# Optimization experiments

Hardware: AMD Instinct MI355X
Metric: run time of the kernel (lower is better)

Reference implementation:

```python
import jax, jax.numpy as jnp
import numpy as np

U, S, D = 4096, 8192, 32
NUM_REGIONS = 128
GA = 0.1


def setup_inputs() -> dict:
    key = jax.random.key(0)
    k1, k2, k3, k4, k5, k6 = jax.random.split(key, 6)
    user_emb = jax.random.normal(k1, (U, D), dtype=jnp.float32) * 0.01
    item_emb = jax.random.normal(k2, (S, D), dtype=jnp.float32) * 0.01
    train_mask = jax.random.randint(k3, (U, S), 0, 2, dtype=jnp.int32)
    true_qos = jax.random.normal(k4, (U, S), dtype=jnp.float32)
    us_lossweight = jax.random.uniform(k5, (U, S), dtype=jnp.float32)
    region_index = jax.random.randint(k6, (U,), 0, NUM_REGIONS, dtype=jnp.int32)
    return {
        "user_emb": user_emb,
        "item_emb": item_emb,
        "train_mask": train_mask,
        "true_qos": true_qos,
        "us_lossweight": us_lossweight,
        "region_index": region_index,
    }


def _region_loss(user_emb, region_index):
    # per-region sums and counts via a single segment reduction
    sums = jax.ops.segment_sum(user_emb, region_index, num_segments=NUM_REGIONS)  # [R, D]
    counts = jax.ops.segment_sum(jnp.ones((user_emb.shape[0],), dtype=user_emb.dtype),
                                 region_index, num_segments=NUM_REGIONS)  # [R]
    cnt = counts[region_index]                      # [U]
    loo_mean = (sums[region_index] - user_emb) / jnp.maximum(cnt - 1.0, 1.0)[:, None]
    dev = jnp.abs(user_emb - loo_mean)              # [U, D]
    # regions with a single user are skipped in the original loop
    valid = (cnt > 1.0)[:, None]
    return jnp.sum(jnp.where(valid, dev, 0.0))


def reference(user_emb, item_emb, train_mask, true_qos, us_lossweight, region_index):
    pre_qos = (user_emb @ item_emb.T) * train_mask.astype(user_emb.dtype)  # [U, S]
    mse = (pre_qos - true_qos) ** 2
    loss = jnp.sum(us_lossweight * mse)
    regionloss = _region_loss(user_emb, region_index)
    return loss + GA * regionloss
```

## Files before the change

kernel.cpp:

```cpp
#include <hip/hip_runtime.h>

#define U 4096
#define S 8192
#define D 32
#define NUM_REGIONS 128
#define GA 0.1f

#define TU 32
#define TI 512
#define THREADS 256
#define LCAP 256


__global__ __launch_bounds__(256) void region_kernel(
    const float* __restrict__ user_emb,
    const int* __restrict__ region_index,
    float* __restrict__ rl_accum) {
    __shared__ int   ridx[U];
    __shared__ int   ulist[LCAP];
    __shared__ int   ucnt;
    __shared__ float part[8][D];
    __shared__ float redsum[D];

    if (threadIdx.x == 0) ucnt = 0;

    #pragma unroll
    for (int i = 0; i < U / 4 / 256; i++)
        ((int4*)ridx)[threadIdx.x + i * 256] =
            ((const int4*)region_index)[threadIdx.x + i * 256];
    __syncthreads();

    const int r = blockIdx.x;

    for (int u = threadIdx.x; u < U; u += 256) {
        if (ridx[u] == r) {
            int p = atomicAdd(&ucnt, 1);
            if (p < LCAP) ulist[p] = u;
        }
    }
    __syncthreads();

    const int n = min(ucnt, LCAP);
    const int d = threadIdx.x & (D - 1);
    const int w = threadIdx.x >> 5;

    float psum = 0.0f;
    for (int i = w; i < n; i += 8)
        psum += user_emb[ulist[i] * D + d];
    part[w][d] = psum;
    __syncthreads();
    if (w == 0) {
        float s = 0.0f;
        #pragma unroll
        for (int i = 0; i < 8; i++) s += part[i][d];
        redsum[d] = s;
    }
    __syncthreads();

    float acc = 0.0f;
    if (n > 1) {
        const float inv = 1.0f / (float)(n - 1);
        const float sd = redsum[d];
        for (int i = w; i < n; i += 8) {
            float e = user_emb[ulist[i] * D + d];
            acc += fabsf(e - (sd - e) * inv);
        }
    }

    #pragma unroll
    for (int off = 32; off > 0; off >>= 1) acc += __shfl_down(acc, off, 64);
    __shared__ float wp[4];
    int lane = threadIdx.x & 63, wid = threadIdx.x >> 6;
    if (lane == 0) wp[wid] = acc;
    __syncthreads();
    if (threadIdx.x == 0)
        atomicAdd(rl_accum, wp[0] + wp[1] + wp[2] + wp[3]);
}


#define PIN4(v) asm volatile("" : "+v"(v.x), "+v"(v.y), "+v"(v.z), "+v"(v.w))

__global__ __attribute__((amdgpu_waves_per_eu(4, 4)))
void mse_kernel(
    const float* __restrict__ user_emb,
    const float* __restrict__ item_emb,
    const int* __restrict__ train_mask,
    const float* __restrict__ true_qos,
    const float* __restrict__ us_lossweight,
    float* __restrict__ loss_accum) {
    __shared__ float uemb[TU][D];

    const int ub = blockIdx.x * TU;
    const int sb = blockIdx.y * TI;

    {
        const float4* src = (const float4*)(user_emb + (size_t)ub * D);
        ((float4*)&uemb[0][0])[threadIdx.x] = src[threadIdx.x];
    }

    const int s0 = sb + 2 * threadIdx.x;

    float4 ir0[8], ir1[8];
    {
        const float4* ip0 = (const float4*)(item_emb + (size_t)s0 * D);
        const float4* ip1 = (const float4*)(item_emb + (size_t)(s0 + 1) * D);
        #pragma unroll
        for (int k = 0; k < 8; k++) { ir0[k] = ip0[k]; ir1[k] = ip1[k]; }
        #pragma unroll
        for (int k = 0; k < 8; k++) { PIN4(ir0[k]); PIN4(ir1[k]); }
    }
    __syncthreads();

    const size_t base0 = (size_t)ub * S + s0;
    int2   m_n = *(const int2*)(train_mask + base0);
    float2 q_n = *(const float2*)(true_qos + base0);
    float2 w_n = *(const float2*)(us_lossweight + base0);

    float acc = 0.0f;
    #pragma unroll 1
    for (int uu = 0; uu < TU; uu++) {
        int2   m = m_n;
        float2 q = q_n;
        float2 w = w_n;
        if (uu + 1 < TU) {
            const size_t nb = base0 + (size_t)(uu + 1) * S;
            m_n = *(const int2*)(train_mask + nb);
            q_n = *(const float2*)(true_qos + nb);
            w_n = *(const float2*)(us_lossweight + nb);
        }

        float d0 = 0.0f, d1 = 0.0f;
        const float4* ur = (const float4*)&uemb[uu][0];
        #pragma unroll
        for (int k = 0; k < 8; k++) {
            float4 uv = ur[k];
            d0 += uv.x * ir0[k].x + uv.y * ir0[k].y + uv.z * ir0[k].z + uv.w * ir0[k].w;
            d1 += uv.x * ir1[k].x + uv.y * ir1[k].y + uv.z * ir1[k].z + uv.w * ir1[k].w;
        }
        float p0 = d0 * (float)m.x;
        float p1 = d1 * (float)m.y;
        float e0 = p0 - q.x;
        float e1 = p1 - q.y;
        acc += w.x * e0 * e0 + w.y * e1 * e1;
    }

    #pragma unroll
    for (int off = 32; off > 0; off >>= 1) acc += __shfl_down(acc, off, 64);
    __shared__ float wp[THREADS / 64];
    int lane = threadIdx.x & 63, wid = threadIdx.x >> 6;
    if (lane == 0) wp[wid] = acc;
    __syncthreads();
    if (threadIdx.x == 0) {
        float t = 0.0f;
        #pragma unroll
        for (int i = 0; i < THREADS / 64; i++) t += wp[i];
        atomicAdd(loss_accum, t);
    }
}

__global__ void finalize_kernel(const float* __restrict__ loss_acc,
                                const float* __restrict__ rl_acc,
                                float* __restrict__ out) {
    out[0] = loss_acc[0] + GA * rl_acc[0];
}

extern "C" void kernel_launch(void* const* d_in, const int* in_sizes, int n_in,
                              void* d_out, int out_size, void* d_ws, size_t ws_size,
                              hipStream_t stream) {
    const float* user_emb      = (const float*)d_in[0];
    const float* item_emb      = (const float*)d_in[1];
    const int*   train_mask    = (const int*)d_in[2];
    const float* true_qos      = (const float*)d_in[3];
    const float* us_lossweight = (const float*)d_in[4];
    const int*   region_index  = (const int*)d_in[5];
    float* out = (float*)d_out;

    float* ws       = (float*)d_ws;
    float* loss_acc = ws;
    float* rl_acc   = ws + 1;
    hipMemsetAsync(d_ws, 0, 2 * sizeof(float), stream);

    region_kernel<<<NUM_REGIONS, 256, 0, stream>>>(user_emb, region_index, rl_acc);

    dim3 grid(U / TU, S / TI);
    mse_kernel<<<grid, THREADS, 0, stream>>>(
        user_emb, item_emb, train_mask, true_qos, us_lossweight, loss_acc);

    finalize_kernel<<<1, 1, 0, stream>>>(loss_acc, rl_acc, out);
}
```

Before: 376.9 us.

## Fuse region loss into MSE kernel and process one item per thread

Merges the region-loss kernel into the MSE kernel: blocks with blockIdx.y==0 (128 of them, one per region since U/TU=128) run the region reduction after their MSE tile, which removes one kernel launch. Each thread now handles a single item instead of two, and TI is halved to keep the grid covering all items. The waves_per_eu(4,4) attribute is replaced by launch_bounds. The fused kernel carries the 16KB ridx shared array in every block, which may reduce occupancy, and the scalar loads replace the earlier int2/float2 vector loads.

```diff
diff --git a/kernel.cpp b/kernel.cpp
--- a/kernel.cpp
+++ b/kernel.cpp
@@ -7,30 +7,102 @@
 #define GA 0.1f
 
 #define TU 32
-#define TI 512
+#define TI 256
 #define THREADS 256
 #define LCAP 256
 
+#define PIN4(v) asm volatile("" : "+v"(v.x), "+v"(v.y), "+v"(v.z), "+v"(v.w))
 
-__global__ __launch_bounds__(256) void region_kernel(
+
+__global__ __launch_bounds__(THREADS) void fused_kernel(
     const float* __restrict__ user_emb,
+    const float* __restrict__ item_emb,
+    const int* __restrict__ train_mask,
+    const float* __restrict__ true_qos,
+    const float* __restrict__ us_lossweight,
     const int* __restrict__ region_index,
+    float* __restrict__ loss_accum,
     float* __restrict__ rl_accum) {
+    __shared__ float uemb[TU][D];
     __shared__ int   ridx[U];
     __shared__ int   ulist[LCAP];
     __shared__ int   ucnt;
     __shared__ float part[8][D];
     __shared__ float redsum[D];
+    __shared__ float wp[THREADS / 64];
+
+    const int ub = blockIdx.x * TU;
+    const int sb = blockIdx.y * TI;
+
+    {
+        const float4* src = (const float4*)(user_emb + (size_t)ub * D);
+        ((float4*)&uemb[0][0])[threadIdx.x] = src[threadIdx.x];
+    }
+
+    const int s0 = sb + threadIdx.x;
+    float4 ir[8];
+    {
+        const float4* ip = (const float4*)(item_emb + (size_t)s0 * D);
+        #pragma unroll
+        for (int k = 0; k < 8; k++) ir[k] = ip[k];
+        #pragma unroll
+        for (int k = 0; k < 8; k++) PIN4(ir[k]);
+    }
+    __syncthreads();
+
+    const size_t base0 = (size_t)ub * S + s0;
+    int   m_n = train_mask[base0];
+    float q_n = true_qos[base0];
+    float w_n = us_lossweight[base0];
+
+    float acc = 0.0f;
+    #pragma unroll 1
+    for (int uu = 0; uu < TU; uu++) {
+        int   m = m_n;
+        float q = q_n;
+        float w = w_n;
+        if (uu + 1 < TU) {
+            const size_t nb = base0 + (size_t)(uu + 1) * S;
+            m_n = train_mask[nb];
+            q_n = true_qos[nb];
+            w_n = us_lossweight[nb];
+        }
+
+        float d0 = 0.0f;
+        const float4* ur = (const float4*)&uemb[uu][0];
+        #pragma unroll
+        for (int k = 0; k < 8; k++) {
+            float4 uv = ur[k];
+            d0 += uv.x * ir[k].x + uv.y * ir[k].y + uv.z * ir[k].z + uv.w * ir[k].w;
+        }
+        float p = d0 * (float)m;
+        float e = p - q;
+        acc += w * e * e;
+    }
+
+    #pragma unroll
+    for (int off = 32; off > 0; off >>= 1) acc += __shfl_down(acc, off, 64);
+    {
+        int lane = threadIdx.x & 63, wid = threadIdx.x >> 6;
+        if (lane == 0) wp[wid] = acc;
+        __syncthreads();
+        if (threadIdx.x == 0) {
+            float t = 0.0f;
+            #pragma unroll
+            for (int i = 0; i < THREADS / 64; i++) t += wp[i];
+            atomicAdd(loss_accum, t);
+        }
+    }
+
+    if (blockIdx.y != 0) return;
+    const int r = blockIdx.x;
 
     if (threadIdx.x == 0) ucnt = 0;
-
     #pragma unroll
     for (int i = 0; i < U / 4 / 256; i++)
         ((int4*)ridx)[threadIdx.x + i * 256] =
             ((const int4*)region_index)[threadIdx.x + i * 256];
     __syncthreads();
-
-    const int r = blockIdx.x;
 
     for (int u = threadIdx.x; u < U; u += 256) {
         if (ridx[u] == r) {
@@ -42,119 +114,43 @@
 
     const int n = min(ucnt, LCAP);
     const int d = threadIdx.x & (D - 1);
-    const int w = threadIdx.x >> 5;
+    const int w8 = threadIdx.x >> 5;
 
     float psum = 0.0f;
-    for (int i = w; i < n; i += 8)
+    for (int i = w8; i < n; i += 8)
         psum += user_emb[ulist[i] * D + d];
-    part[w][d] = psum;
+    part[w8][d] = psum;
     __syncthreads();
-    if (w == 0) {
-        float s = 0.0f;
+    if (w8 == 0) {
+        float sum = 0.0f;
         #pragma unroll
-        for (int i = 0; i < 8; i++) s += part[i][d];
-        redsum[d] = s;
+        for (int i = 0; i < 8; i++) sum += part[i][d];
+        redsum[d] = sum;
     }
     __syncthreads();
 
-    float acc = 0.0f;
+    float racc = 0.0f;
     if (n > 1) {
         const float inv = 1.0f / (float)(n - 1);
         const float sd = redsum[d];
-        for (int i = w; i < n; i += 8) {
+        for (int i = w8; i < n; i += 8) {
             float e = user_emb[ulist[i] * D + d];
-            acc += fabsf(e - (sd - e) * inv);
+            racc += fabsf(e - (sd - e) * inv);
         }
     }
 
     #pragma unroll
-    for (int off = 32; off > 0; off >>= 1) acc += __shfl_down(acc, off, 64);
-    __shared__ float wp[4];
-    int lane = threadIdx.x & 63, wid = threadIdx.x >> 6;
-    if (lane == 0) wp[wid] = acc;
-    __syncthreads();
-    if (threadIdx.x == 0)
-        atomicAdd(rl_accum, wp[0] + wp[1] + wp[2] + wp[3]);
-}
-
-
-#define PIN4(v) asm volatile("" : "+v"(v.x), "+v"(v.y), "+v"(v.z), "+v"(v.w))
-
-__global__ __attribute__((amdgpu_waves_per_eu(4, 4)))
-void mse_kernel(
-    const float* __restrict__ user_emb,
-    const float* __restrict__ item_emb,
-    const int* __restrict__ train_mask,
-    const float* __restrict__ true_qos,
-    const float* __restrict__ us_lossweight,
-    float* __restrict__ loss_accum) {
-    __shared__ float uemb[TU][D];
-
-    const int ub = blockIdx.x * TU;
-    const int sb = blockIdx.y * TI;
-
+    for (int off = 32; off > 0; off >>= 1) racc += __shfl_down(racc, off, 64);
     {
-        const float4* src = (const float4*)(user_emb + (size_t)ub * D);
-        ((float4*)&uemb[0][0])[threadIdx.x] = src[threadIdx.x];
-    }
-
-    const int s0 = sb + 2 * threadIdx.x;
-
-    float4 ir0[8], ir1[8];
-    {
-        const float4* ip0 = (const float4*)(item_emb + (size_t)s0 * D);
-        const float4* ip1 = (const float4*)(item_emb + (size_t)(s0 + 1) * D);
-        #pragma unroll
-        for (int k = 0; k < 8; k++) { ir0[k] = ip0[k]; ir1[k] = ip1[k]; }
-        #pragma unroll
-        for (int k = 0; k < 8; k++) { PIN4(ir0[k]); PIN4(ir1[k]); }
-    }
-    __syncthreads();
-
-    const size_t base0 = (size_t)ub * S + s0;
-    int2   m_n = *(const int2*)(train_mask + base0);
-    float2 q_n = *(const float2*)(true_qos + base0);
-    float2 w_n = *(const float2*)(us_lossweight + base0);
-
-    float acc = 0.0f;
-    #pragma unroll 1
-    for (int uu = 0; uu < TU; uu++) {
-        int2   m = m_n;
-        float2 q = q_n;
-        float2 w = w_n;
-        if (uu + 1 < TU) {
-            const size_t nb = base0 + (size_t)(uu + 1) * S;
-            m_n = *(const int2*)(train_mask + nb);
-            q_n = *(const float2*)(true_qos + nb);
-            w_n = *(const float2*)(us_lossweight + nb);
+        int lane = threadIdx.x & 63, wid = threadIdx.x >> 6;
+        if (lane == 0) wp[wid] = racc;
+        __syncthreads();
+        if (threadIdx.x == 0) {
+            float t = 0.0f;
+            #pragma unroll
+            for (int i = 0; i < THREADS / 64; i++) t += wp[i];
+            atomicAdd(rl_accum, t);
         }
-
-        float d0 = 0.0f, d1 = 0.0f;
-        const float4* ur = (const float4*)&uemb[uu][0];
-        #pragma unroll
-        for (int k = 0; k < 8; k++) {
-            float4 uv = ur[k];
-            d0 += uv.x * ir0[k].x + uv.y * ir0[k].y + uv.z * ir0[k].z + uv.w * ir0[k].w;
-            d1 += uv.x * ir1[k].x + uv.y * ir1[k].y + uv.z * ir1[k].z + uv.w * ir1[k].w;
-        }
-        float p0 = d0 * (float)m.x;
-        float p1 = d1 * (float)m.y;
-        float e0 = p0 - q.x;
-        float e1 = p1 - q.y;
-        acc += w.x * e0 * e0 + w.y * e1 * e1;
-    }
-
-    #pragma unroll
-    for (int off = 32; off > 0; off >>= 1) acc += __shfl_down(acc, off, 64);
-    __shared__ float wp[THREADS / 64];
-    int lane = threadIdx.x & 63, wid = threadIdx.x >> 6;
-    if (lane == 0) wp[wid] = acc;
-    __syncthreads();
-    if (threadIdx.x == 0) {
-        float t = 0.0f;
-        #pragma unroll
-        for (int i = 0; i < THREADS / 64; i++) t += wp[i];
-        atomicAdd(loss_accum, t);
     }
 }
 
@@ -180,11 +176,10 @@
     float* rl_acc   = ws + 1;
     hipMemsetAsync(d_ws, 0, 2 * sizeof(float), stream);
 
-    region_kernel<<<NUM_REGIONS, 256, 0, stream>>>(user_emb, region_index, rl_acc);
-
     dim3 grid(U / TU, S / TI);
-    mse_kernel<<<grid, THREADS, 0, stream>>>(
-        user_emb, item_emb, train_mask, true_qos, us_lossweight, loss_acc);
+    fused_kernel<<<grid, THREADS, 0, stream>>>(
+        user_emb, item_emb, train_mask, true_qos, us_lossweight, region_index,
+        loss_acc, rl_acc);
 
     finalize_kernel<<<1, 1, 0, stream>>>(loss_acc, rl_acc, out);
 }
```

Result: no change. 383.7 us (+1.8%).
